# Optimization experiments

Hardware: AMD Instinct MI355X
Metric: run time of the kernel (lower is better)

## Reference

```python
import math
import jax, jax.numpy as jnp
import numpy as np

D_MODEL = 1024
HEADS = 16
D_K = D_MODEL // HEADS
BATCH = 4
SEQ = 2048


def setup_inputs() -> dict:
    key = jax.random.key(0)
    ks = jax.random.split(key, 7)
    q = jax.random.normal(ks[0], (BATCH, SEQ, D_MODEL), dtype=jnp.float32)
    k = jax.random.normal(ks[1], (BATCH, SEQ, D_MODEL), dtype=jnp.float32)
    v = jax.random.normal(ks[2], (BATCH, SEQ, D_MODEL), dtype=jnp.float32)
    # causal mask: True = masked (filled with -inf), broadcastable over batch & heads
    mask = jnp.triu(jnp.ones((SEQ, SEQ), dtype=bool), k=1)[None, None, :, :]
    s = 1.0 / math.sqrt(D_MODEL)
    Wq = jax.random.normal(ks[3], (D_MODEL, D_MODEL), dtype=jnp.float32) * s
    Wk = jax.random.normal(ks[4], (D_MODEL, D_MODEL), dtype=jnp.float32) * s
    Wv = jax.random.normal(ks[5], (D_MODEL, D_MODEL), dtype=jnp.float32) * s
    Wo = jax.random.normal(ks[6], (D_MODEL, D_MODEL), dtype=jnp.float32) * s
    return {"q": q, "k": k, "v": v, "mask": mask, "Wq": Wq, "Wk": Wk, "Wv": Wv, "Wo": Wo}


def reference(q, k, v, mask, Wq, Wk, Wv, Wo):
    B, S, _ = q.shape
    # Linear(d_model, d_model, bias=False): y = x @ W.T
    def proj(x, W):
        return (x @ W.T).reshape(B, S, HEADS, D_K).transpose(0, 2, 1, 3)  # [B,H,S,Dk]
    qh, kh, vh = proj(q, Wq), proj(k, Wk), proj(v, Wv)
    scores = jnp.einsum('bhqd,bhkd->bhqk', qh, kh) / math.sqrt(D_K)
    scores = jnp.where(mask, -jnp.inf, scores)
    attn = jax.nn.softmax(scores, axis=-1)  # dropout p=0 is identity
    ctx = jnp.einsum('bhqk,bhkd->bhqd', attn, vh)
    ctx = ctx.transpose(0, 2, 1, 3).reshape(B, S, D_MODEL)
    return ctx @ Wo.T
```

## Files before the change

### kernel.cpp

```cpp
#include <hip/hip_runtime.h>
#include <hip/hip_bf16.h>
#include <stdint.h>

#define S_LEN 2048
#define DMODEL 1024
#define HEADS 16
#define DK 64
#define LDK 72

#define QSCALE 0.18033688011112042f

typedef __attribute__((ext_vector_type(8))) short bf16x8;
typedef __attribute__((ext_vector_type(4))) float f32x4;

__device__ __forceinline__ unsigned short f2bf(float f) {
    union { float f; unsigned u; } c; c.f = f;
    unsigned u = c.u;
    u += 0x7fffu + ((u >> 16) & 1u);
    return (unsigned short)(u >> 16);
}

__device__ __forceinline__ unsigned pkbf(float a, float b) {
    union { float f; unsigned u; } ca, cb; ca.f = a; cb.f = b;
    unsigned ua = ca.u + (0x7fffu + ((ca.u >> 16) & 1u));
    unsigned ub = cb.u + (0x7fffu + ((cb.u >> 16) & 1u));
    return __builtin_amdgcn_perm(ub, ua, 0x07060302);
}

__device__ __forceinline__ unsigned cvtpk(float a, float b) {
    unsigned r;
    asm("v_cvt_pk_bf16_f32 %0, %1, %2" : "=v"(r) : "v"(a), "v"(b));
    return r;
}

__device__ __forceinline__ void g2lds16(const unsigned short* g, unsigned short* l) {
    __builtin_amdgcn_global_load_lds((const __attribute__((address_space(1))) void*)g,
                                     (__attribute__((address_space(3))) void*)l, 16, 0, 0);
}

__global__ __launch_bounds__(256) void convert_kernel(
    const float* __restrict__ q, const float* __restrict__ k, const float* __restrict__ v,
    const float* __restrict__ Wq, const float* __restrict__ Wk, const float* __restrict__ Wv,
    const float* __restrict__ Wo,
    unsigned short* __restrict__ qbf, unsigned short* __restrict__ kbf,
    unsigned short* __restrict__ vbf, unsigned short* __restrict__ wbf)
{
    const float* src; unsigned short* dst; int n8;
    const int y = blockIdx.y;
    if (y == 0)      { src = q;  dst = qbf;           n8 = 1048576; }
    else if (y == 1) { src = k;  dst = kbf;           n8 = 1048576; }
    else if (y == 2) { src = v;  dst = vbf;           n8 = 1048576; }
    else if (y == 3) { src = Wq; dst = wbf;           n8 = 131072; }
    else if (y == 4) { src = Wk; dst = wbf + 1048576; n8 = 131072; }
    else if (y == 5) { src = Wv; dst = wbf + 2097152; n8 = 131072; }
    else             { src = Wo; dst = wbf + 3145728; n8 = 131072; }
    int i = blockIdx.x * 256 + threadIdx.x;
    if (i >= n8) return;
    float4 f0 = ((const float4*)src)[(size_t)2 * i];
    float4 f1 = ((const float4*)src)[(size_t)2 * i + 1];
    union { unsigned u[4]; uint4 v; } o;
    o.u[0] = pkbf(f0.x, f0.y); o.u[1] = pkbf(f0.z, f0.w);
    o.u[2] = pkbf(f1.x, f1.y); o.u[3] = pkbf(f1.z, f1.w);
    *(uint4*)&dst[(size_t)8 * i] = o.v;
}

__global__ __launch_bounds__(256) void proj_gemm_kernel(
    const unsigned short* __restrict__ qbf, const unsigned short* __restrict__ kbf,
    const unsigned short* __restrict__ vbf, const unsigned short* __restrict__ wbf,
    unsigned short* __restrict__ qh, unsigned short* __restrict__ kh,
    unsigned short* __restrict__ vh_t)
{
    const unsigned short* A; const unsigned short* Bm; unsigned short* Y;
    const int z = blockIdx.z;
    if (z == 0)      { A = qbf; Bm = wbf;           Y = qh;   }
    else if (z == 1) { A = kbf; Bm = wbf + 1048576; Y = kh;   }
    else             { A = vbf; Bm = wbf + 2097152; Y = vh_t; }

    __shared__ unsigned short sA[128 * 64];
    __shared__ unsigned short sB[128 * 64];

    const int t    = threadIdx.x;
    const int lane = t & 63;
    const int wid  = t >> 6;
    const int wrow = (wid >> 1) * 64;
    const int wcol = (wid & 1) * 64;
    const int m0   = blockIdx.x * 128;
    const int n0   = blockIdx.y * 128;
    const int lrow = lane & 15;
    const int quad = lane >> 4;
    const int lk   = quad * 8;

    const unsigned short* gA = A + (size_t)(m0 + wid * 32 + (lane >> 3)) * 1024 + (lane & 7) * 8;
    const unsigned short* gB = Bm + (size_t)(n0 + wid * 32 + (lane >> 3)) * 1024 + (lane & 7) * 8;
    unsigned short* lA = sA + wid * 2048;
    unsigned short* lB = sB + wid * 2048;

    f32x4 acc[4][4];
    for (int i = 0; i < 4; i++) for (int j = 0; j < 4; j++) acc[i][j] = (f32x4){0.f, 0.f, 0.f, 0.f};

    for (int kb = 0; kb < 1024; kb += 64) {
        __syncthreads();
        for (int it = 0; it < 4; ++it) {
            g2lds16(gA + (size_t)it * 8 * 1024, lA + it * 512);
            g2lds16(gB + (size_t)it * 8 * 1024, lB + it * 512);
        }
        gA += 64; gB += 64;
        __syncthreads();
        for (int kk = 0; kk < 64; kk += 32) {
            bf16x8 a[4], b[4];
            for (int i = 0; i < 4; i++) a[i] = *(const bf16x8*)&sA[(wrow + i * 16 + lrow) * 64 + kk + lk];
            for (int j = 0; j < 4; j++) b[j] = *(const bf16x8*)&sB[(wcol + j * 16 + lrow) * 64 + kk + lk];
            for (int i = 0; i < 4; i++)
                for (int j = 0; j < 4; j++)
                    acc[i][j] = __builtin_amdgcn_mfma_f32_16x16x32_bf16(a[i], b[j], acc[i][j], 0, 0, 0);
        }
    }

    const float scale = (z == 0) ? QSCALE : 1.0f;
    for (int i = 0; i < 4; i++) {
        int grow = m0 + wrow + i * 16 + quad * 4;
        for (int j = 0; j < 4; j++) {
            int gcol = n0 + wcol + j * 16 + lrow;
            int h = gcol >> 6, d = gcol & 63;
            for (int r = 0; r < 4; r++) {
                int row = grow + r;
                int b_ = row >> 11;
                int s_ = row & 2047;
                unsigned short val = f2bf(acc[i][j][r] * scale);
                if (z == 2)
                    Y[(((size_t)(b_ * HEADS + h) * DK) + d) * S_LEN + s_] = val;
                else
                    Y[(((size_t)(b_ * HEADS + h) * S_LEN) + s_) * DK + d] = val;
            }
        }
    }
}

__global__ __launch_bounds__(256) void outproj_gemm_kernel(
    const unsigned short* __restrict__ ctx, const unsigned short* __restrict__ wobf,
    float* __restrict__ out)
{
    __shared__ unsigned short sA[128 * 64];
    __shared__ unsigned short sB[128 * 64];

    const int t    = threadIdx.x;
    const int lane = t & 63;
    const int wid  = t >> 6;
    const int wrow = (wid >> 1) * 64;
    const int wcol = (wid & 1) * 64;
    const int m0   = blockIdx.x * 128;
    const int n0   = blockIdx.y * 128;
    const int lrow = lane & 15;
    const int quad = lane >> 4;
    const int lk   = quad * 8;

    const unsigned short* gA = ctx  + (size_t)(m0 + wid * 32 + (lane >> 3)) * 1024 + (lane & 7) * 8;
    const unsigned short* gB = wobf + (size_t)(n0 + wid * 32 + (lane >> 3)) * 1024 + (lane & 7) * 8;
    unsigned short* lA = sA + wid * 2048;
    unsigned short* lB = sB + wid * 2048;

    f32x4 acc[4][4];
    for (int i = 0; i < 4; i++) for (int j = 0; j < 4; j++) acc[i][j] = (f32x4){0.f, 0.f, 0.f, 0.f};

    for (int kb = 0; kb < 1024; kb += 64) {
        __syncthreads();
        for (int it = 0; it < 4; ++it) {
            g2lds16(gA + (size_t)it * 8 * 1024, lA + it * 512);
            g2lds16(gB + (size_t)it * 8 * 1024, lB + it * 512);
        }
        gA += 64; gB += 64;
        __syncthreads();
        for (int kk = 0; kk < 64; kk += 32) {
            bf16x8 a[4], b[4];
            for (int i = 0; i < 4; i++) a[i] = *(const bf16x8*)&sA[(wrow + i * 16 + lrow) * 64 + kk + lk];
            for (int j = 0; j < 4; j++) b[j] = *(const bf16x8*)&sB[(wcol + j * 16 + lrow) * 64 + kk + lk];
            for (int i = 0; i < 4; i++)
                for (int j = 0; j < 4; j++)
                    acc[i][j] = __builtin_amdgcn_mfma_f32_16x16x32_bf16(a[i], b[j], acc[i][j], 0, 0, 0);
        }
    }

    for (int i = 0; i < 4; i++) {
        int grow = m0 + wrow + i * 16 + quad * 4;
        for (int j = 0; j < 4; j++) {
            int gcol = n0 + wcol + j * 16 + lrow;
            for (int r = 0; r < 4; r++)
                out[(size_t)(grow + r) * DMODEL + gcol] = acc[i][j][r];
        }
    }
}

__global__ __launch_bounds__(256) void attn_kernel(
    const unsigned short* __restrict__ qh, const unsigned short* __restrict__ kh,
    const unsigned short* __restrict__ vh_t, unsigned short* __restrict__ ctx)
{
    __shared__ unsigned short sK[64 * LDK];
    __shared__ unsigned short sVt[64 * LDK];
    __shared__ unsigned short sPT[4][32 * LDK];

    const int t    = threadIdx.x;
    const int lane = t & 63;
    const int wid  = t >> 6;
    const int lin  = (int)(blockIdx.y * gridDim.x + blockIdx.x);
    const int wlin = (lin & 7) * 64 + (lin >> 3);
    const int qx   = wlin & 7;
    const int bh   = wlin >> 3;
    const size_t base = (size_t)bh * S_LEN * DK;
    const int lrow = lane & 15;
    const int quad = lane >> 4;
    const int b_ = bh >> 4, h_ = bh & 15;
    unsigned short* myPT = &sPT[wid][0];

    const int sr0 = t >> 3;
    const int sc0 = (t & 7) * 8;
    const unsigned short* gK = kh + base;
    const unsigned short* gV = vh_t + base;

    for (int pass = 0; pass < 2; ++pass) {
        const int qt = pass ? (15 - qx) : qx;
        const int q0 = qt * 128;
        const int qw0 = q0 + wid * 32;

        bf16x8 qreg[2][2];
        for (int nf = 0; nf < 2; ++nf)
            for (int h = 0; h < 2; ++h)
                qreg[nf][h] = *(const bf16x8*)&qh[base + (size_t)(qw0 + nf * 16 + lrow) * DK + h * 32 + quad * 8];

        f32x4 o[4][2];
        for (int mf = 0; mf < 4; mf++) for (int nf = 0; nf < 2; nf++) o[mf][nf] = (f32x4){0.f, 0.f, 0.f, 0.f};
        float lstat[2] = { 0.f, 0.f };

        const int ntiles = q0 / 64 + 2;

        uint4 rK0 = *(const uint4*)&gK[(size_t)sr0 * DK + sc0];
        uint4 rK1 = *(const uint4*)&gK[(size_t)(sr0 + 32) * DK + sc0];
        uint4 rV0 = *(const uint4*)&gV[(size_t)sr0 * S_LEN + sc0];
        uint4 rV1 = *(const uint4*)&gV[(size_t)(sr0 + 32) * S_LEN + sc0];

        for (int kt = 0; kt < ntiles; ++kt) {
            const int k0 = kt * 64;
            __syncthreads();
            *(uint4*)&sK [sr0 * LDK + sc0]        = rK0;
            *(uint4*)&sK [(sr0 + 32) * LDK + sc0] = rK1;
            *(uint4*)&sVt[sr0 * LDK + sc0]        = rV0;
            *(uint4*)&sVt[(sr0 + 32) * LDK + sc0] = rV1;
            if (kt + 1 < ntiles) {
                const int kn = k0 + 64;
                rK0 = *(const uint4*)&gK[(size_t)(kn + sr0) * DK + sc0];
                rK1 = *(const uint4*)&gK[(size_t)(kn + sr0 + 32) * DK + sc0];
                rV0 = *(const uint4*)&gV[(size_t)sr0 * S_LEN + kn + sc0];
                rV1 = *(const uint4*)&gV[(size_t)(sr0 + 32) * S_LEN + kn + sc0];
            }
            __syncthreads();

            if (k0 > qw0 + 31) continue;

            f32x4 st[4][2];
            for (int mf = 0; mf < 4; mf++) for (int nf = 0; nf < 2; nf++) st[mf][nf] = (f32x4){0.f, 0.f, 0.f, 0.f};
            for (int h = 0; h < 2; ++h) {
                bf16x8 kf[4];
                for (int mf = 0; mf < 4; mf++)
                    kf[mf] = *(const bf16x8*)&sK[(mf * 16 + lrow) * LDK + h * 32 + quad * 8];
                __builtin_amdgcn_s_setprio(1);
                for (int mf = 0; mf < 4; mf++)
                    for (int nf = 0; nf < 2; nf++)
                        st[mf][nf] = __builtin_amdgcn_mfma_f32_16x16x32_bf16(kf[mf], qreg[nf][h], st[mf][nf], 0, 0, 0);
                __builtin_amdgcn_s_setprio(0);
            }

            const bool need_mask = (k0 + 63 > qw0);

            for (int nf = 0; nf < 2; ++nf) {
                const int qidx = qw0 + nf * 16 + lrow;
                if (need_mask) {
                    for (int mf = 0; mf < 4; mf++)
                        for (int r = 0; r < 4; r++) {
                            int key = k0 + mf * 16 + quad * 4 + r;
                            if (key > qidx) st[mf][nf][r] = -INFINITY;
                        }
                }
                float rsum = 0.f;
                for (int mf = 0; mf < 4; mf++) {
                    float p0 = exp2f(st[mf][nf][0]);
                    float p1 = exp2f(st[mf][nf][1]);
                    float p2 = exp2f(st[mf][nf][2]);
                    float p3 = exp2f(st[mf][nf][3]);
                    rsum += (p0 + p1) + (p2 + p3);
                    uint2 pk;
                    pk.x = cvtpk(p0, p1);
                    pk.y = cvtpk(p2, p3);
                    *(uint2*)&myPT[(nf * 16 + lrow) * LDK + mf * 16 + quad * 4] = pk;
                }
                lstat[nf] += rsum;
            }

            for (int h = 0; h < 2; ++h) {
                bf16x8 vf[4], pf[2];
                for (int mf = 0; mf < 4; mf++)
                    vf[mf] = *(const bf16x8*)&sVt[(mf * 16 + lrow) * LDK + h * 32 + quad * 8];
                for (int nf = 0; nf < 2; nf++)
                    pf[nf] = *(const bf16x8*)&myPT[(nf * 16 + lrow) * LDK + h * 32 + quad * 8];
                __builtin_amdgcn_s_setprio(1);
                for (int mf = 0; mf < 4; mf++)
                    for (int nf = 0; nf < 2; nf++)
                        o[mf][nf] = __builtin_amdgcn_mfma_f32_16x16x32_bf16(vf[mf], pf[nf], o[mf][nf], 0, 0, 0);
                __builtin_amdgcn_s_setprio(0);
            }
        }

        for (int nf = 0; nf < 2; ++nf) {
            float ls = lstat[nf];
            ls += __shfl_xor(ls, 16);
            ls += __shfl_xor(ls, 32);
            float inv = 1.f / ls;
            int s_ = qw0 + nf * 16 + lrow;
            size_t rowbase = (((size_t)(b_ * S_LEN + s_)) * HEADS + h_) * DK;
            for (int mf = 0; mf < 4; mf++) {
                int d0 = mf * 16 + quad * 4;
                uint2 pk;
                pk.x = pkbf(o[mf][nf][0] * inv, o[mf][nf][1] * inv);
                pk.y = pkbf(o[mf][nf][2] * inv, o[mf][nf][3] * inv);
                *(uint2*)&ctx[rowbase + d0] = pk;
            }
        }
    }
}

__global__ __launch_bounds__(256) void proj_fb_kernel(
    const float* __restrict__ q, const float* __restrict__ k, const float* __restrict__ v,
    const float* __restrict__ Wq, const float* __restrict__ Wk, const float* __restrict__ Wv,
    unsigned short* __restrict__ qh, unsigned short* __restrict__ kh, unsigned short* __restrict__ vh_t)
{
    const float* X; const float* W; unsigned short* Y;
    if (blockIdx.z == 0)      { X = q; W = Wq; Y = qh; }
    else if (blockIdx.z == 1) { X = k; W = Wk; Y = kh; }
    else                      { X = v; W = Wv; Y = vh_t; }

    __shared__ short sA[128 * LDK];
    __shared__ short sB[128 * LDK];
    const int t = threadIdx.x, lane = t & 63, wid = t >> 6;
    const int wrow = (wid >> 1) * 64, wcol = (wid & 1) * 64;
    const int m0 = blockIdx.x * 128, n0 = blockIdx.y * 128;
    const int lrow = lane & 15, quad = lane >> 4, lk = quad * 8;

    f32x4 acc[4][4];
    for (int i = 0; i < 4; i++) for (int j = 0; j < 4; j++) acc[i][j] = (f32x4){0.f, 0.f, 0.f, 0.f};

    for (int kb = 0; kb < DMODEL; kb += 64) {
        for (int it = 0; it < 8; ++it) {
            int idx = t + it * 256;
            int row = idx >> 4, c4 = (idx & 15) * 4;
            float4 fa = *(const float4*)&X[(size_t)(m0 + row) * DMODEL + kb + c4];
            float4 fb = *(const float4*)&W[(size_t)(n0 + row) * DMODEL + kb + c4];
            short4 sa = { (short)f2bf(fa.x), (short)f2bf(fa.y), (short)f2bf(fa.z), (short)f2bf(fa.w) };
            short4 sb = { (short)f2bf(fb.x), (short)f2bf(fb.y), (short)f2bf(fb.z), (short)f2bf(fb.w) };
            *(short4*)&sA[row * LDK + c4] = sa;
            *(short4*)&sB[row * LDK + c4] = sb;
        }
        __syncthreads();
        for (int kk = 0; kk < 64; kk += 32) {
            bf16x8 a[4], b[4];
            for (int i = 0; i < 4; i++) a[i] = *(const bf16x8*)&sA[(wrow + i * 16 + lrow) * LDK + kk + lk];
            for (int j = 0; j < 4; j++) b[j] = *(const bf16x8*)&sB[(wcol + j * 16 + lrow) * LDK + kk + lk];
            for (int i = 0; i < 4; i++)
                for (int j = 0; j < 4; j++)
                    acc[i][j] = __builtin_amdgcn_mfma_f32_16x16x32_bf16(a[i], b[j], acc[i][j], 0, 0, 0);
        }
        __syncthreads();
    }

    const float scale = (blockIdx.z == 0) ? QSCALE : 1.0f;
    for (int i = 0; i < 4; i++) {
        int grow = m0 + wrow + i * 16 + quad * 4;
        for (int j = 0; j < 4; j++) {
            int gcol = n0 + wcol + j * 16 + lrow;
            int h = gcol >> 6, d = gcol & 63;
            for (int r = 0; r < 4; r++) {
                int row = grow + r, b_ = row >> 11, s_ = row & 2047;
                unsigned short val = f2bf(acc[i][j][r] * scale);
                if (blockIdx.z == 2)
                    Y[(((size_t)(b_ * HEADS + h) * DK) + d) * S_LEN + s_] = val;
                else
                    Y[(((size_t)(b_ * HEADS + h) * S_LEN) + s_) * DK + d] = val;
            }
        }
    }
}

__global__ __launch_bounds__(256) void outproj_fb_kernel(
    const unsigned short* __restrict__ ctx, const float* __restrict__ Wo, float* __restrict__ out)
{
    __shared__ short sA[128 * LDK];
    __shared__ short sB[128 * LDK];
    const int t = threadIdx.x, lane = t & 63, wid = t >> 6;
    const int wrow = (wid >> 1) * 64, wcol = (wid & 1) * 64;
    const int m0 = blockIdx.x * 128, n0 = blockIdx.y * 128;
    const int lrow = lane & 15, quad = lane >> 4, lk = quad * 8;

    f32x4 acc[4][4];
    for (int i = 0; i < 4; i++) for (int j = 0; j < 4; j++) acc[i][j] = (f32x4){0.f, 0.f, 0.f, 0.f};

    for (int kb = 0; kb < DMODEL; kb += 64) {
        for (int it = 0; it < 4; ++it) {
            int idx = t + it * 256;
            int row = idx >> 3, c8 = (idx & 7) * 8;
            *(uint4*)&sA[row * LDK + c8] = *(const uint4*)&ctx[(size_t)(m0 + row) * DMODEL + kb + c8];
        }
        for (int it = 0; it < 8; ++it) {
            int idx = t + it * 256;
            int row = idx >> 4, c4 = (idx & 15) * 4;
            float4 fb = *(const float4*)&Wo[(size_t)(n0 + row) * DMODEL + kb + c4];
            short4 sb = { (short)f2bf(fb.x), (short)f2bf(fb.y), (short)f2bf(fb.z), (short)f2bf(fb.w) };
            *(short4*)&sB[row * LDK + c4] = sb;
        }
        __syncthreads();
        for (int kk = 0; kk < 64; kk += 32) {
            bf16x8 a[4], b[4];
            for (int i = 0; i < 4; i++) a[i] = *(const bf16x8*)&sA[(wrow + i * 16 + lrow) * LDK + kk + lk];
            for (int j = 0; j < 4; j++) b[j] = *(const bf16x8*)&sB[(wcol + j * 16 + lrow) * LDK + kk + lk];
            for (int i = 0; i < 4; i++)
                for (int j = 0; j < 4; j++)
                    acc[i][j] = __builtin_amdgcn_mfma_f32_16x16x32_bf16(a[i], b[j], acc[i][j], 0, 0, 0);
        }
        __syncthreads();
    }

    for (int i = 0; i < 4; i++) {
        int grow = m0 + wrow + i * 16 + quad * 4;
        for (int j = 0; j < 4; j++) {
            int gcol = n0 + wcol + j * 16 + lrow;
            for (int r = 0; r < 4; r++)
                out[(size_t)(grow + r) * DMODEL + gcol] = acc[i][j][r];
        }
    }
}

extern "C" void kernel_launch(void* const* d_in, const int* in_sizes, int n_in,
                              void* d_out, int out_size, void* d_ws, size_t ws_size,
                              hipStream_t stream)
{
    const float* q  = (const float*)d_in[0];
    const float* k  = (const float*)d_in[1];
    const float* v  = (const float*)d_in[2];
    const float* Wq = (const float*)d_in[4];
    const float* Wk = (const float*)d_in[5];
    const float* Wv = (const float*)d_in[6];
    const float* Wo = (const float*)d_in[7];
    float* out = (float*)d_out;

    const size_t M8 = (size_t)8 * 1024 * 1024;
    const size_t need = (size_t)(52) * 1024 * 1024 * 2;

    if (ws_size >= need) {
        unsigned short* qbf  = (unsigned short*)d_ws;
        unsigned short* kbf  = qbf + M8;
        unsigned short* vbf  = kbf + M8;
        unsigned short* wbf  = vbf + M8;
        unsigned short* qh   = wbf + (size_t)4 * 1024 * 1024;
        unsigned short* kh   = qh + M8;
        unsigned short* vh_t = kh + M8;
        unsigned short* ctx  = qbf;

        dim3 gCvt(4096, 7);
        convert_kernel<<<gCvt, 256, 0, stream>>>(q, k, v, Wq, Wk, Wv, Wo, qbf, kbf, vbf, wbf);

        dim3 gProj(64, 8, 3);
        proj_gemm_kernel<<<gProj, 256, 0, stream>>>(qbf, kbf, vbf, wbf, qh, kh, vh_t);

        dim3 gAttn(8, 64);
        attn_kernel<<<gAttn, 256, 0, stream>>>(qh, kh, vh_t, ctx);

        dim3 gOut(64, 8);
        outproj_gemm_kernel<<<gOut, 256, 0, stream>>>(ctx, wbf + (size_t)3 * 1024 * 1024, out);
    } else {
        unsigned short* qh   = (unsigned short*)d_ws;
        unsigned short* kh   = qh + M8;
        unsigned short* vh_t = kh + M8;
        unsigned short* ctx  = vh_t + M8;

        dim3 gProj(64, 8, 3);
        proj_fb_kernel<<<gProj, 256, 0, stream>>>(q, k, v, Wq, Wk, Wv, qh, kh, vh_t);

        dim3 gAttn(8, 64);
        attn_kernel<<<gAttn, 256, 0, stream>>>(qh, kh, vh_t, ctx);

        dim3 gOut(64, 8);
        outproj_fb_kernel<<<gOut, 256, 0, stream>>>(ctx, Wo, out);
    }
}
```

Before: 344.7 us.

## Double-buffer projection GEMMs with 256x128 tiles and swizzled LDS

Replaces the projection and output GEMM inner loops with a shared core that uses 512-thread blocks computing 256x128 tiles. Global-to-LDS loads for the next k-tile are double-buffered so they overlap the current MFMA work, with vmcnt waits in place of two syncthreads per step. LDS columns are XOR-swizzled to avoid bank conflicts, and MFMA issue priority is raised. This costs 96KB of LDS per block, which limits occupancy, and halves the grid size, which may leave fewer blocks to spread across CUs.

Result: faster. 326.8 us (-5.2%).

```diff
diff --git a/kernel.cpp b/kernel.cpp
--- a/kernel.cpp
+++ b/kernel.cpp
@@ -64,7 +64,80 @@
     *(uint4*)&dst[(size_t)8 * i] = o.v;
 }
 
-__global__ __launch_bounds__(256) void proj_gemm_kernel(
+__device__ __forceinline__ void gemm_core_256x128(
+    const unsigned short* __restrict__ Apanel,
+    const unsigned short* __restrict__ Bpanel,
+    unsigned short* sm,
+    f32x4 acc[4][4])
+{
+    const int t    = threadIdx.x;
+    const int lane = t & 63;
+    const int w    = t >> 6;
+    const int wm   = w >> 1;
+    const int wn   = w & 1;
+    const int lrow = lane & 15;
+    const int quad = lane >> 4;
+
+    const int l8   = lane >> 3;
+    const int c16s = (lane & 7) ^ l8;
+    const unsigned short* gA = Apanel + (size_t)(w * 8 + l8) * 1024 + c16s * 8;
+    const unsigned short* gB = Bpanel + (size_t)(w * 8 + l8) * 1024 + c16s * 8;
+    unsigned short* lA = sm + w * 512;
+    unsigned short* lB = sm + 16384 + w * 512;
+
+#define STAGE_KT(bufsel, kt) do {                                         \
+        unsigned short* la = lA + (bufsel) * 24576;                       \
+        unsigned short* lb = lB + (bufsel) * 24576;                       \
+        const unsigned short* ga = gA + (kt) * 64;                        \
+        const unsigned short* gb = gB + (kt) * 64;                        \
+        g2lds16(ga,                        la);                           \
+        g2lds16(ga + (size_t) 64 * 1024,   la + 4096);                    \
+        g2lds16(ga + (size_t)128 * 1024,   la + 8192);                    \
+        g2lds16(ga + (size_t)192 * 1024,   la + 12288);                   \
+        g2lds16(gb,                        lb);                           \
+        g2lds16(gb + (size_t) 64 * 1024,   lb + 4096);                    \
+    } while (0)
+
+    for (int i = 0; i < 4; i++) for (int j = 0; j < 4; j++) acc[i][j] = (f32x4){0.f, 0.f, 0.f, 0.f};
+
+    STAGE_KT(0, 0);
+
+#pragma unroll 1
+    for (int kt = 0; kt < 16; ++kt) {
+        const int buf = kt & 1;
+        if (kt < 15) {
+            STAGE_KT(buf ^ 1, kt + 1);
+            asm volatile("s_waitcnt vmcnt(6)" ::: "memory");
+        } else {
+            asm volatile("s_waitcnt vmcnt(0)" ::: "memory");
+        }
+        __builtin_amdgcn_sched_barrier(0);
+        __builtin_amdgcn_s_barrier();
+        __builtin_amdgcn_sched_barrier(0);
+
+        const unsigned short* tA = sm + buf * 24576;
+        const unsigned short* tB = sm + buf * 24576 + 16384;
+        for (int kh = 0; kh < 2; ++kh) {
+            const int cs = ((kh * 4 + quad) ^ (lrow & 7)) * 8;
+            bf16x8 a[4], b[4];
+            for (int mi = 0; mi < 4; mi++)
+                a[mi] = *(const bf16x8*)&tA[(wm * 64 + mi * 16 + lrow) * 64 + cs];
+            for (int nj = 0; nj < 4; nj++)
+                b[nj] = *(const bf16x8*)&tB[(wn * 64 + nj * 16 + lrow) * 64 + cs];
+            __builtin_amdgcn_s_setprio(1);
+            for (int mi = 0; mi < 4; mi++)
+                for (int nj = 0; nj < 4; nj++)
+                    acc[mi][nj] = __builtin_amdgcn_mfma_f32_16x16x32_bf16(a[mi], b[nj], acc[mi][nj], 0, 0, 0);
+            __builtin_amdgcn_s_setprio(0);
+        }
+        __builtin_amdgcn_sched_barrier(0);
+        __builtin_amdgcn_s_barrier();
+        __builtin_amdgcn_sched_barrier(0);
+    }
+#undef STAGE_KT
+}
+
+__global__ __launch_bounds__(512, 2) void proj_gemm_kernel(
     const unsigned short* __restrict__ qbf, const unsigned short* __restrict__ kbf,
     const unsigned short* __restrict__ vbf, const unsigned short* __restrict__ wbf,
     unsigned short* __restrict__ qh, unsigned short* __restrict__ kh,
@@ -76,51 +149,22 @@
     else if (z == 1) { A = kbf; Bm = wbf + 1048576; Y = kh;   }
     else             { A = vbf; Bm = wbf + 2097152; Y = vh_t; }
 
-    __shared__ unsigned short sA[128 * 64];
-    __shared__ unsigned short sB[128 * 64];
-
-    const int t    = threadIdx.x;
-    const int lane = t & 63;
-    const int wid  = t >> 6;
-    const int wrow = (wid >> 1) * 64;
-    const int wcol = (wid & 1) * 64;
-    const int m0   = blockIdx.x * 128;
-    const int n0   = blockIdx.y * 128;
-    const int lrow = lane & 15;
-    const int quad = lane >> 4;
-    const int lk   = quad * 8;
-
-    const unsigned short* gA = A + (size_t)(m0 + wid * 32 + (lane >> 3)) * 1024 + (lane & 7) * 8;
-    const unsigned short* gB = Bm + (size_t)(n0 + wid * 32 + (lane >> 3)) * 1024 + (lane & 7) * 8;
-    unsigned short* lA = sA + wid * 2048;
-    unsigned short* lB = sB + wid * 2048;
+    __shared__ unsigned short sm[49152];
+
+    const int m0 = blockIdx.x * 256;
+    const int n0 = blockIdx.y * 128;
 
     f32x4 acc[4][4];
-    for (int i = 0; i < 4; i++) for (int j = 0; j < 4; j++) acc[i][j] = (f32x4){0.f, 0.f, 0.f, 0.f};
-
-    for (int kb = 0; kb < 1024; kb += 64) {
-        __syncthreads();
-        for (int it = 0; it < 4; ++it) {
-            g2lds16(gA + (size_t)it * 8 * 1024, lA + it * 512);
-            g2lds16(gB + (size_t)it * 8 * 1024, lB + it * 512);
-        }
-        gA += 64; gB += 64;
-        __syncthreads();
-        for (int kk = 0; kk < 64; kk += 32) {
-            bf16x8 a[4], b[4];
-            for (int i = 0; i < 4; i++) a[i] = *(const bf16x8*)&sA[(wrow + i * 16 + lrow) * 64 + kk + lk];
-            for (int j = 0; j < 4; j++) b[j] = *(const bf16x8*)&sB[(wcol + j * 16 + lrow) * 64 + kk + lk];
-            for (int i = 0; i < 4; i++)
-                for (int j = 0; j < 4; j++)
-                    acc[i][j] = __builtin_amdgcn_mfma_f32_16x16x32_bf16(a[i], b[j], acc[i][j], 0, 0, 0);
-        }
-    }
-
+    gemm_core_256x128(A + (size_t)m0 * 1024, Bm + (size_t)n0 * 1024, sm, acc);
+
+    const int t = threadIdx.x, lane = t & 63;
+    const int wm = (t >> 6) >> 1, wn = (t >> 6) & 1;
+    const int lrow = lane & 15, quad = lane >> 4;
     const float scale = (z == 0) ? QSCALE : 1.0f;
     for (int i = 0; i < 4; i++) {
-        int grow = m0 + wrow + i * 16 + quad * 4;
+        int grow = m0 + wm * 64 + i * 16 + quad * 4;
         for (int j = 0; j < 4; j++) {
-            int gcol = n0 + wcol + j * 16 + lrow;
+            int gcol = n0 + wn * 64 + j * 16 + lrow;
             int h = gcol >> 6, d = gcol & 63;
             for (int r = 0; r < 4; r++) {
                 int row = grow + r;
@@ -136,54 +180,25 @@
     }
 }
 
-__global__ __launch_bounds__(256) void outproj_gemm_kernel(
+__global__ __launch_bounds__(512, 2) void outproj_gemm_kernel(
     const unsigned short* __restrict__ ctx, const unsigned short* __restrict__ wobf,
     float* __restrict__ out)
 {
-    __shared__ unsigned short sA[128 * 64];
-    __shared__ unsigned short sB[128 * 64];
-
-    const int t    = threadIdx.x;
-    const int lane = t & 63;
-    const int wid  = t >> 6;
-    const int wrow = (wid >> 1) * 64;
-    const int wcol = (wid & 1) * 64;
-    const int m0   = blockIdx.x * 128;
-    const int n0   = blockIdx.y * 128;
-    const int lrow = lane & 15;
-    const int quad = lane >> 4;
-    const int lk   = quad * 8;
-
-    const unsigned short* gA = ctx  + (size_t)(m0 + wid * 32 + (lane >> 3)) * 1024 + (lane & 7) * 8;
-    const unsigned short* gB = wobf + (size_t)(n0 + wid * 32 + (lane >> 3)) * 1024 + (lane & 7) * 8;
-    unsigned short* lA = sA + wid * 2048;
-    unsigned short* lB = sB + wid * 2048;
+    __shared__ unsigned short sm[49152];
+
+    const int m0 = blockIdx.x * 256;
+    const int n0 = blockIdx.y * 128;
 
     f32x4 acc[4][4];
-    for (int i = 0; i < 4; i++) for (int j = 0; j < 4; j++) acc[i][j] = (f32x4){0.f, 0.f, 0.f, 0.f};
-
-    for (int kb = 0; kb < 1024; kb += 64) {
-        __syncthreads();
-        for (int it = 0; it < 4; ++it) {
-            g2lds16(gA + (size_t)it * 8 * 1024, lA + it * 512);
-            g2lds16(gB + (size_t)it * 8 * 1024, lB + it * 512);
-        }
-        gA += 64; gB += 64;
-        __syncthreads();
-        for (int kk = 0; kk < 64; kk += 32) {
-            bf16x8 a[4], b[4];
-            for (int i = 0; i < 4; i++) a[i] = *(const bf16x8*)&sA[(wrow + i * 16 + lrow) * 64 + kk + lk];
-            for (int j = 0; j < 4; j++) b[j] = *(const bf16x8*)&sB[(wcol + j * 16 + lrow) * 64 + kk + lk];
-            for (int i = 0; i < 4; i++)
-                for (int j = 0; j < 4; j++)
-                    acc[i][j] = __builtin_amdgcn_mfma_f32_16x16x32_bf16(a[i], b[j], acc[i][j], 0, 0, 0);
-        }
-    }
-
+    gemm_core_256x128(ctx + (size_t)m0 * 1024, wobf + (size_t)n0 * 1024, sm, acc);
+
+    const int t = threadIdx.x, lane = t & 63;
+    const int wm = (t >> 6) >> 1, wn = (t >> 6) & 1;
+    const int lrow = lane & 15, quad = lane >> 4;
     for (int i = 0; i < 4; i++) {
-        int grow = m0 + wrow + i * 16 + quad * 4;
+        int grow = m0 + wm * 64 + i * 16 + quad * 4;
         for (int j = 0; j < 4; j++) {
-            int gcol = n0 + wcol + j * 16 + lrow;
+            int gcol = n0 + wn * 64 + j * 16 + lrow;
             for (int r = 0; r < 4; r++)
                 out[(size_t)(grow + r) * DMODEL + gcol] = acc[i][j][r];
         }
@@ -464,14 +479,14 @@
         dim3 gCvt(4096, 7);
         convert_kernel<<<gCvt, 256, 0, stream>>>(q, k, v, Wq, Wk, Wv, Wo, qbf, kbf, vbf, wbf);
 
-        dim3 gProj(64, 8, 3);
-        proj_gemm_kernel<<<gProj, 256, 0, stream>>>(qbf, kbf, vbf, wbf, qh, kh, vh_t);
+        dim3 gProj(32, 8, 3);
+        proj_gemm_kernel<<<gProj, 512, 0, stream>>>(qbf, kbf, vbf, wbf, qh, kh, vh_t);
 
         dim3 gAttn(8, 64);
         attn_kernel<<<gAttn, 256, 0, stream>>>(qh, kh, vh_t, ctx);
 
-        dim3 gOut(64, 8);
-        outproj_gemm_kernel<<<gOut, 256, 0, stream>>>(ctx, wbf + (size_t)3 * 1024 * 1024, out);
+        dim3 gOut(32, 8);
+        outproj_gemm_kernel<<<gOut, 512, 0, stream>>>(ctx, wbf + (size_t)3 * 1024 * 1024, out);
     } else {
         unsigned short* qh   = (unsigned short*)d_ws;
         unsigned short* kh   = qh + M8;
```
